# Optimization experiments

Measured on AMD Instinct MI355X. Metric: run time of the kernel, lower is better.

## Reference

```python
import jax, jax.numpy as jnp
import numpy as np

B, S, D, H = 4, 2048, 512, 8
EPS = 1e-5

def _layer_norm(x, gamma, beta):
    mu = jnp.mean(x, axis=-1, keepdims=True)
    var = jnp.mean(jnp.square(x - mu), axis=-1, keepdims=True)
    return (x - mu) * jax.lax.rsqrt(var + EPS) * gamma + beta

def setup_inputs() -> dict:
    key = jax.random.key(0)
    ks = jax.random.split(key, 6)
    sc = 1.0 / np.sqrt(D)
    return {
        "seq_k": jax.random.normal(ks[0], (B, S, D), jnp.float32),
        "seq_q": jax.random.normal(ks[1], (B, S, D), jnp.float32),
        "seq_v": jax.random.normal(ks[2], (B, S, D), jnp.float32),
        "W1": jax.random.normal(ks[3], (D, D), jnp.float32) * sc,
        "W2": jax.random.normal(ks[4], (D, D), jnp.float32) * sc,
        "W3": jax.random.normal(ks[5], (D, D), jnp.float32) * sc,
        "gamma": jnp.ones((D,), jnp.float32),
        "beta": jnp.zeros((D,), jnp.float32),
    }

def reference(seq_k, seq_q, seq_v, W1, W2, W3, gamma, beta):
    # is_layer_norm=True: pre-LN on values; seq_v_value is the normed v
    v_in = _layer_norm(seq_v, gamma, beta)
    # nn.Linear(bias=False): y = x @ W^T
    q = seq_q @ W1.T
    k = seq_k @ W2.T
    v = v_in @ W3.T
    hd = D // H
    q = q.reshape(B, S, H, hd).transpose(0, 2, 1, 3)  # b h s d
    k = k.reshape(B, S, H, hd).transpose(0, 2, 1, 3)
    v = v.reshape(B, S, H, hd).transpose(0, 2, 1, 3)
    # faithful quirk: scores = K @ Q^T, unscaled
    scores = jnp.einsum("bhid,bhjd->bhij", k, q)  # b h s s
    attn = jax.nn.softmax(scores, axis=-1)
    out = jnp.einsum("bhij,bhjd->bhid", attn, v)  # b h s d
    out = out.transpose(0, 2, 1, 3).reshape(B, S, D)
    out = out + v_in                 # is_residual=True
    return _layer_norm(out, gamma, beta)  # final LN
```

## Files before the change

### kernel.cpp

```cpp
#include <hip/hip_runtime.h>
#include <math.h>

#define BB 4
#define SS 2048
#define DD 512
#define HH 8
#define HD 64
#define NTOK (BB*SS)
#define EPS 1e-5f
#define NE ((size_t)NTOK * DD)
#define WN ((size_t)DD * DD)
#define LOG2E 1.4426950408889634f

typedef _Float16 half8v __attribute__((ext_vector_type(8)));
typedef _Float16 half4v __attribute__((ext_vector_type(4)));
typedef _Float16 half2v __attribute__((ext_vector_type(2)));
typedef float f32x4 __attribute__((ext_vector_type(4)));

__device__ __forceinline__ float fast_exp2(float x) {
#if __has_builtin(__builtin_amdgcn_exp2f)
    return __builtin_amdgcn_exp2f(x);
#else
    return __expf(x * 0.6931471805599453f);
#endif
}

__device__ __forceinline__ half2v pack2(float a, float b) {
    return __builtin_bit_cast(half2v, __builtin_amdgcn_cvt_pkrtz(a, b));
}

__device__ __forceinline__ half4v pack4(float a, float b, float c, float d) {
    half2v lo = pack2(a, b);
    half2v hi = pack2(c, d);
    half4v r; r[0] = lo[0]; r[1] = lo[1]; r[2] = hi[0]; r[3] = hi[1];
    return r;
}

__device__ __forceinline__ void gload_lds16(const void* g, void* l) {
    __builtin_amdgcn_global_load_lds(
        (const __attribute__((address_space(1))) unsigned int*)g,
        (__attribute__((address_space(3))) unsigned int*)l, 16, 0, 0);
}

__global__ __launch_bounds__(256) void ln_kernel(const float* __restrict__ x,
                                                 const float* __restrict__ res,
                                                 const float* __restrict__ gamma,
                                                 const float* __restrict__ beta,
                                                 float* __restrict__ y) {
    int row = blockIdx.x;
    const float* xr = x + (size_t)row * DD;
    int t = threadIdx.x;
    float2 v = ((const float2*)xr)[t];
    {
        float2 r = ((const float2*)(res + (size_t)row * DD))[t];
        v.x += r.x; v.y += r.y;
    }
    float s = v.x + v.y;
    float ss = v.x * v.x + v.y * v.y;
    #pragma unroll
    for (int off = 32; off; off >>= 1) {
        s  += __shfl_down(s,  off);
        ss += __shfl_down(ss, off);
    }
    __shared__ float ws0[4], ws1[4];
    int wid = t >> 6, lane = t & 63;
    if (lane == 0) { ws0[wid] = s; ws1[wid] = ss; }
    __syncthreads();
    __shared__ float mu_s, rstd_s;
    if (t == 0) {
        float S0 = ws0[0] + ws0[1] + ws0[2] + ws0[3];
        float S1 = ws1[0] + ws1[1] + ws1[2] + ws1[3];
        float mu = S0 * (1.0f / DD);
        float var = S1 * (1.0f / DD) - mu * mu;
        mu_s = mu;
        rstd_s = rsqrtf(var + EPS);
    }
    __syncthreads();
    float mu = mu_s, rstd = rstd_s;
    float2 g = ((const float2*)gamma)[t];
    float2 bb = ((const float2*)beta)[t];
    float2 o;
    o.x = (v.x - mu) * rstd * g.x + bb.x;
    o.y = (v.y - mu) * rstd * g.y + bb.y;
    ((float2*)(y + (size_t)row * DD))[t] = o;
}

__global__ __launch_bounds__(256) void prep_kernel(const float* __restrict__ seq_v,
                                                   const float* __restrict__ seq_q,
                                                   const float* __restrict__ seq_k,
                                                   const float* __restrict__ W1,
                                                   const float* __restrict__ W2,
                                                   const float* __restrict__ W3,
                                                   const float* __restrict__ gamma,
                                                   const float* __restrict__ beta,
                                                   float* __restrict__ v_in,
                                                   _Float16* __restrict__ v16,
                                                   _Float16* __restrict__ qk16,
                                                   _Float16* __restrict__ w16) {
    int bid = blockIdx.x;
    int t = threadIdx.x;
    if (bid < NTOK) {
        int row = bid;
        float2 v = ((const float2*)(seq_v + (size_t)row * DD))[t];
        float s = v.x + v.y;
        float ss = v.x * v.x + v.y * v.y;
        #pragma unroll
        for (int off = 32; off; off >>= 1) {
            s  += __shfl_down(s,  off);
            ss += __shfl_down(ss, off);
        }
        __shared__ float ws0[4], ws1[4];
        int wid = t >> 6, lane = t & 63;
        if (lane == 0) { ws0[wid] = s; ws1[wid] = ss; }
        __syncthreads();
        __shared__ float mu_s, rstd_s;
        if (t == 0) {
            float S0 = ws0[0] + ws0[1] + ws0[2] + ws0[3];
            float S1 = ws1[0] + ws1[1] + ws1[2] + ws1[3];
            float mu = S0 * (1.0f / DD);
            float var = S1 * (1.0f / DD) - mu * mu;
            mu_s = mu;
            rstd_s = rsqrtf(var + EPS);
        }
        __syncthreads();
        float mu = mu_s, rstd = rstd_s;
        float2 g = ((const float2*)gamma)[t];
        float2 bb = ((const float2*)beta)[t];
        float2 o;
        o.x = (v.x - mu) * rstd * g.x + bb.x;
        o.y = (v.y - mu) * rstd * g.y + bb.y;
        ((float2*)(v_in + (size_t)row * DD))[t] = o;
        *(half2v*)&v16[(size_t)row * DD + 2 * t] = pack2(o.x, o.y);
    } else if (bid < 2 * NTOK) {
        size_t i = ((size_t)(bid - NTOK) * 256 + t) * 4;
        const float* src = (i < NE) ? (seq_q + i) : (seq_k + (i - NE));
        float4 v = *(const float4*)src;
        *(half4v*)(qk16 + i) = pack4(v.x, v.y, v.z, v.w);
    } else {
        size_t i = ((size_t)(bid - 2 * NTOK) * 256 + t) * 4;
        const float* src; float sc;
        if (i < WN)          { src = W1 + i;            sc = LOG2E; }
        else if (i < 2 * WN) { src = W2 + (i - WN);     sc = 1.0f; }
        else                 { src = W3 + (i - 2 * WN); sc = 1.0f; }
        float4 v = *(const float4*)src;
        *(half4v*)(w16 + i) = pack4(v.x * sc, v.y * sc, v.z * sc, v.w * sc);
    }
}

#define GBM 128
#define GBN 128
#define GBK 64
__global__ __launch_bounds__(256) void gemm_mfma(const _Float16* __restrict__ Aall,
                                                 const _Float16* __restrict__ Wall,
                                                 _Float16* __restrict__ Call,
                                                 _Float16* __restrict__ vtOut) {
    __shared__ __align__(16) _Float16 smem[GBM * GBN];
    _Float16* As = smem;
    _Float16* Ws = smem + (size_t)GBM * GBK;
    int z = blockIdx.z;
    bool isv = (z == 2);
    const _Float16* A = Aall + (size_t)z * NE;
    const _Float16* W = Wall + (size_t)z * WN;
    int t = threadIdx.x, w = t >> 6, lane = t & 63, q = lane >> 4, ln = lane & 15;
    int lrow = lane >> 3, lseg = lane & 7;
    int m0 = blockIdx.y * GBM, n0 = blockIdx.x * GBN;
    int wm = w & 1, wn = w >> 1;
    f32x4 acc[4][4];
    #pragma unroll
    for (int mt = 0; mt < 4; ++mt)
        #pragma unroll
        for (int nt = 0; nt < 4; ++nt)
            acc[mt][nt] = (f32x4){0.f, 0.f, 0.f, 0.f};

    int gs = lseg ^ lrow;
    for (int k0 = 0; k0 < DD; k0 += GBK) {
        #pragma unroll
        for (int p = 0; p < 4; ++p) {
            int r = w * 32 + p * 8 + lrow;
            gload_lds16(A + (size_t)(m0 + r) * DD + k0 + gs * 8,
                        As + (size_t)(w * 32 + p * 8) * GBK);
            gload_lds16(W + (size_t)(n0 + r) * DD + k0 + gs * 8,
                        Ws + (size_t)(w * 32 + p * 8) * GBK);
        }
        __syncthreads();
        #pragma unroll
        for (int kk = 0; kk < 2; ++kk) {
            int ch = ((4 * kk + q) ^ (ln & 7)) * 8;
            half8v af[4], wf[4];
            #pragma unroll
            for (int mt = 0; mt < 4; ++mt)
                af[mt] = *(half8v*)&As[(wm * 64 + mt * 16 + ln) * GBK + ch];
            #pragma unroll
            for (int nt = 0; nt < 4; ++nt)
                wf[nt] = *(half8v*)&Ws[(wn * 64 + nt * 16 + ln) * GBK + ch];
            if (!isv) {
                #pragma unroll
                for (int mt = 0; mt < 4; ++mt)
                    #pragma unroll
                    for (int nt = 0; nt < 4; ++nt)
                        acc[mt][nt] = __builtin_amdgcn_mfma_f32_16x16x32_f16(
                            wf[nt], af[mt], acc[mt][nt], 0, 0, 0);
            } else {
                #pragma unroll
                for (int mt = 0; mt < 4; ++mt)
                    #pragma unroll
                    for (int nt = 0; nt < 4; ++nt)
                        acc[mt][nt] = __builtin_amdgcn_mfma_f32_16x16x32_f16(
                            af[mt], wf[nt], acc[mt][nt], 0, 0, 0);
            }
        }
        __syncthreads();
    }

    if (!isv) {
        #pragma unroll
        for (int mt = 0; mt < 4; ++mt) {
            int mloc = wm * 64 + mt * 16 + ln;
            #pragma unroll
            for (int nt = 0; nt < 4; ++nt) {
                int nloc = wn * 64 + nt * 16 + q * 4;
                int cs = (nloc >> 3) ^ (mloc & 7);
                char* p = (char*)smem + mloc * 256 + cs * 16 + (nloc & 7) * 2;
                *(half4v*)p = pack4(acc[mt][nt][0], acc[mt][nt][1],
                                    acc[mt][nt][2], acc[mt][nt][3]);
            }
        }
    } else {
        #pragma unroll
        for (int nt = 0; nt < 4; ++nt) {
            int dloc = wn * 64 + nt * 16 + ln;
            #pragma unroll
            for (int mt = 0; mt < 4; ++mt) {
                int sloc = wm * 64 + mt * 16 + q * 4;
                int cs = (sloc >> 3) ^ (dloc & 7);
                char* p = (char*)smem + dloc * 256 + cs * 16 + (sloc & 7) * 2;
                *(half4v*)p = pack4(acc[mt][nt][0], acc[mt][nt][1],
                                    acc[mt][nt][2], acc[mt][nt][3]);
            }
        }
    }
    __syncthreads();
    int bq = m0 >> 11, sbase = m0 & (SS - 1);
    if (!isv) {
        _Float16* C = Call + (size_t)z * NE;
        #pragma unroll
        for (int p = 0; p < 8; ++p) {
            int id = p * 256 + t;
            int r = id >> 4, c = id & 15;
            half8v vv = *(half8v*)((char*)smem + r * 256 + ((c ^ (r & 7)) * 16));
            int n = n0 + c * 8;
            int h = n >> 6, d0 = n & 63;
            *(half8v*)&C[((size_t)(bq * HH + h) * SS + (sbase + r)) * HD + d0] = vv;
        }
    } else {
        #pragma unroll
        for (int p = 0; p < 8; ++p) {
            int id = p * 256 + t;
            int r = id >> 4, c = id & 15;
            half8v vv = *(half8v*)((char*)smem + r * 256 + ((c ^ (r & 7)) * 16));
            int d = n0 + r;
            int h = d >> 6, dd = d & 63;
            *(half8v*)&vtOut[((size_t)(bq * HH + h) * HD + dd) * SS + sbase + c * 8] = vv;
        }
    }
}

#define AI 128
#define AJ 64
__global__ __launch_bounds__(512, 4) void attn_mfma(const _Float16* __restrict__ qh,
                                                    const _Float16* __restrict__ kh,
                                                    const _Float16* __restrict__ vt,
                                                    float* __restrict__ out) {
    __shared__ __align__(16) _Float16 Qt[2][AJ * HD];
    __shared__ __align__(16) _Float16 Vs[2][HD * AJ];
    __shared__ __align__(16) _Float16 Ps[AI * AJ];
    int t = threadIdx.x, w = t >> 6, lane = t & 63, q = lane >> 4, ln = lane & 15;
    int wg = blockIdx.x;
    int slot = wg >> 3;
    int bh = (wg & 7) * 4 + (slot >> 4);
    int i0 = (slot & 15) * AI;
    int b = bh >> 3, h = bh & 7;
    const _Float16* Kb = kh + (size_t)bh * SS * HD;
    const _Float16* Qb = qh + (size_t)bh * SS * HD;
    const _Float16* Vb = vt + (size_t)bh * HD * SS;

    half8v kf[2];
    #pragma unroll
    for (int kk = 0; kk < 2; ++kk)
        kf[kk] = *(const half8v*)&Kb[(size_t)(i0 + w * 16 + ln) * HD + kk * 32 + q * 8];

    f32x4 oacc[4], lacc;
    float m_run = -3.0e38f;
    lacc = (f32x4){0.f, 0.f, 0.f, 0.f};
    #pragma unroll
    for (int mtd = 0; mtd < 4; ++mtd) oacc[mtd] = (f32x4){0.f, 0.f, 0.f, 0.f};
    half8v ones;
    #pragma unroll
    for (int e = 0; e < 8; ++e) ones[e] = (_Float16)1.0f;
    const f32x4 zf = (f32x4){0.f, 0.f, 0.f, 0.f};

    int sr = t >> 3;
    int sc = t & 7;
    int ssw = sc ^ (sr & 7);

    gload_lds16(Qb + (size_t)sr * HD + ssw * 8, &Qt[0][(size_t)w * 512]);
    gload_lds16(Vb + (size_t)sr * SS + ssw * 8, &Vs[0][(size_t)w * 512]);

    const int NITER = SS / AJ;
    for (int jt = 0; jt < NITER; ++jt) {
        int cur = jt & 1;
        __syncthreads();

        if (jt + 1 < NITER) {
            int j1 = (jt + 1) * AJ;
            gload_lds16(Qb + (size_t)(j1 + sr) * HD + ssw * 8, &Qt[cur ^ 1][(size_t)w * 512]);
            gload_lds16(Vb + (size_t)sr * SS + j1 + ssw * 8,   &Vs[cur ^ 1][(size_t)w * 512]);
        }

        f32x4 sacc[4];
        __builtin_amdgcn_s_setprio(1);
        #pragma unroll
        for (int mt = 0; mt < 4; ++mt) {
            half8v qf = *(half8v*)&Qt[cur][(mt * 16 + ln) * HD + (q ^ (ln & 7)) * 8];
            sacc[mt] = __builtin_amdgcn_mfma_f32_16x16x32_f16(qf, kf[0], zf, 0, 0, 0);
        }
        #pragma unroll
        for (int mt = 0; mt < 4; ++mt) {
            half8v qf = *(half8v*)&Qt[cur][(mt * 16 + ln) * HD + ((4 + q) ^ (ln & 7)) * 8];
            sacc[mt] = __builtin_amdgcn_mfma_f32_16x16x32_f16(qf, kf[1], sacc[mt], 0, 0, 0);
        }
        __builtin_amdgcn_s_setprio(0);

        float mx = fmaxf(fmaxf(sacc[0][0], sacc[0][1]), fmaxf(sacc[0][2], sacc[0][3]));
        #pragma unroll
        for (int mt = 1; mt < 4; ++mt) {
            float m2 = fmaxf(fmaxf(sacc[mt][0], sacc[mt][1]),
                             fmaxf(sacc[mt][2], sacc[mt][3]));
            mx = fmaxf(mx, m2);
        }
        mx = fmaxf(mx, __shfl_xor(mx, 16));
        mx = fmaxf(mx, __shfl_xor(mx, 32));
        if (__any(mx > m_run + 7.0f)) {
            float mn = fmaxf(m_run, mx);
            float a = fast_exp2(m_run - mn);
            lacc *= a;
            #pragma unroll
            for (int mtd = 0; mtd < 4; ++mtd) oacc[mtd] *= a;
            m_run = mn;
        }

        int rp = w * 16 + ln;
        #pragma unroll
        for (int mt = 0; mt < 4; ++mt) {
            float p0 = fast_exp2(sacc[mt][0] - m_run);
            float p1 = fast_exp2(sacc[mt][1] - m_run);
            float p2 = fast_exp2(sacc[mt][2] - m_run);
            float p3 = fast_exp2(sacc[mt][3] - m_run);
            int cw = mt * 2 + (q >> 1);
            int pos = cw ^ (ln & 7);
            *(half4v*)&Ps[(size_t)rp * AJ + pos * 8 + (q & 1) * 4] =
                pack4(p0, p1, p2, p3);
        }

        __builtin_amdgcn_s_setprio(1);
        #pragma unroll
        for (int ks = 0; ks < 2; ++ks) {
            int pos = ((ks * 4 + q) ^ (ln & 7)) * 8;
            half8v pf = *(half8v*)&Ps[(size_t)(w * 16 + ln) * AJ + pos];
            lacc = __builtin_amdgcn_mfma_f32_16x16x32_f16(ones, pf, lacc, 0, 0, 0);
            #pragma unroll
            for (int mtd = 0; mtd < 4; ++mtd) {
                half8v vf = *(half8v*)&Vs[cur][(size_t)(mtd * 16 + ln) * AJ + pos];
                oacc[mtd] = __builtin_amdgcn_mfma_f32_16x16x32_f16(vf, pf, oacc[mtd], 0, 0, 0);
            }
        }
        __builtin_amdgcn_s_setprio(0);
    }

    float inv = 1.0f / lacc[0];
    int i = i0 + w * 16 + ln;
    #pragma unroll
    for (int mtd = 0; mtd < 4; ++mtd) {
        float4 o;
        o.x = oacc[mtd][0] * inv;
        o.y = oacc[mtd][1] * inv;
        o.z = oacc[mtd][2] * inv;
        o.w = oacc[mtd][3] * inv;
        *(float4*)&out[(size_t)(b * SS + i) * DD + h * HD + mtd * 16 + q * 4] = o;
    }
}

extern "C" void kernel_launch(void* const* d_in, const int* in_sizes, int n_in,
                              void* d_out, int out_size, void* d_ws, size_t ws_size,
                              hipStream_t stream) {
    const float* seq_k = (const float*)d_in[0];
    const float* seq_q = (const float*)d_in[1];
    const float* seq_v = (const float*)d_in[2];
    const float* W1    = (const float*)d_in[3];
    const float* W2    = (const float*)d_in[4];
    const float* W3    = (const float*)d_in[5];
    const float* gamma = (const float*)d_in[6];
    const float* beta  = (const float*)d_in[7];
    float* out = (float*)d_out;

    const size_t MB = 1024 * 1024;
    char* w8 = (char*)d_ws;
    float*    v_in = (float*)w8;
    _Float16* a16  = (_Float16*)(w8 + 16 * MB);
    _Float16* w16  = (_Float16*)(w8 + 40 * MB);
    _Float16* qh   = (_Float16*)(w8 + 48 * MB);
    _Float16* vt   = (_Float16*)(w8 + 64 * MB);
    float*    ao   = (float*)(w8 + 16 * MB);

    _Float16* q16 = a16;
    _Float16* v16 = a16 + 2 * NE;
    _Float16* kh  = qh + NE;

    hipLaunchKernelGGL(prep_kernel, dim3(2 * NTOK + 768), dim3(256), 0, stream,
                       seq_v, seq_q, seq_k, W1, W2, W3, gamma, beta,
                       v_in, v16, q16, w16);
    hipLaunchKernelGGL(gemm_mfma, dim3(DD / GBN, NTOK / GBM, 3), dim3(256), 0, stream,
                       a16, w16, qh, vt);
    hipLaunchKernelGGL(attn_mfma, dim3((SS / AI) * BB * HH), dim3(512), 0, stream,
                       qh, kh, vt, ao);
    hipLaunchKernelGGL(ln_kernel, dim3(NTOK), dim3(256), 0, stream,
                       ao, v_in, gamma, beta, out);
}
```

Before: 197.9 us.

## Double-buffer GEMM LDS tiles and remap blocks per XCD

The QKV projection GEMM now double-buffers its LDS tiles. It issues the next k-tile's async global-to-LDS loads before computing on the current one, which cuts the loop to one barrier per iteration. It also raises wave priority around the MFMA section. The 3D grid is flattened into a 1D grid and remapped so that the blocks running on each XCD share A-row tiles, aiming for better L2 reuse. LDS use grows to two stage buffers, and the epilogue reuses buffer 0, so correctness depends on the barrier ordering.

```diff
diff --git a/kernel.cpp b/kernel.cpp
--- a/kernel.cpp
+++ b/kernel.cpp
@@ -154,16 +154,19 @@
                                                  const _Float16* __restrict__ Wall,
                                                  _Float16* __restrict__ Call,
                                                  _Float16* __restrict__ vtOut) {
-    __shared__ __align__(16) _Float16 smem[GBM * GBN];
-    _Float16* As = smem;
-    _Float16* Ws = smem + (size_t)GBM * GBK;
-    int z = blockIdx.z;
+    __shared__ __align__(16) _Float16 smem[2][2 * GBM * GBK];
+    int wg = blockIdx.x;
+    int local = wg >> 3;
+    int z = local >> 5;
+    int r5 = local & 31;
+    int my = (wg & 7) * 8 + (r5 >> 2);
+    int nx = r5 & 3;
     bool isv = (z == 2);
     const _Float16* A = Aall + (size_t)z * NE;
     const _Float16* W = Wall + (size_t)z * WN;
     int t = threadIdx.x, w = t >> 6, lane = t & 63, q = lane >> 4, ln = lane & 15;
     int lrow = lane >> 3, lseg = lane & 7;
-    int m0 = blockIdx.y * GBM, n0 = blockIdx.x * GBN;
+    int m0 = my * GBM, n0 = nx * GBN;
     int wm = w & 1, wn = w >> 1;
     f32x4 acc[4][4];
     #pragma unroll
@@ -173,26 +176,39 @@
             acc[mt][nt] = (f32x4){0.f, 0.f, 0.f, 0.f};
 
     int gs = lseg ^ lrow;
-    for (int k0 = 0; k0 < DD; k0 += GBK) {
+
+    auto stage = [&](int k0, int buf) {
+        _Float16* Asb = smem[buf];
+        _Float16* Wsb = smem[buf] + GBM * GBK;
         #pragma unroll
         for (int p = 0; p < 4; ++p) {
-            int r = w * 32 + p * 8 + lrow;
-            gload_lds16(A + (size_t)(m0 + r) * DD + k0 + gs * 8,
-                        As + (size_t)(w * 32 + p * 8) * GBK);
-            gload_lds16(W + (size_t)(n0 + r) * DD + k0 + gs * 8,
-                        Ws + (size_t)(w * 32 + p * 8) * GBK);
-        }
+            int rr = w * 32 + p * 8 + lrow;
+            gload_lds16(A + (size_t)(m0 + rr) * DD + k0 + gs * 8,
+                        Asb + (size_t)(w * 32 + p * 8) * GBK);
+            gload_lds16(W + (size_t)(n0 + rr) * DD + k0 + gs * 8,
+                        Wsb + (size_t)(w * 32 + p * 8) * GBK);
+        }
+    };
+
+    stage(0, 0);
+    const int NK = DD / GBK;
+    for (int ki = 0; ki < NK; ++ki) {
+        int cur = ki & 1;
         __syncthreads();
+        if (ki + 1 < NK) stage((ki + 1) * GBK, cur ^ 1);
+        _Float16* Asb = smem[cur];
+        _Float16* Wsb = smem[cur] + GBM * GBK;
+        __builtin_amdgcn_s_setprio(1);
         #pragma unroll
         for (int kk = 0; kk < 2; ++kk) {
             int ch = ((4 * kk + q) ^ (ln & 7)) * 8;
             half8v af[4], wf[4];
             #pragma unroll
             for (int mt = 0; mt < 4; ++mt)
-                af[mt] = *(half8v*)&As[(wm * 64 + mt * 16 + ln) * GBK + ch];
+                af[mt] = *(half8v*)&Asb[(wm * 64 + mt * 16 + ln) * GBK + ch];
             #pragma unroll
             for (int nt = 0; nt < 4; ++nt)
-                wf[nt] = *(half8v*)&Ws[(wn * 64 + nt * 16 + ln) * GBK + ch];
+                wf[nt] = *(half8v*)&Wsb[(wn * 64 + nt * 16 + ln) * GBK + ch];
             if (!isv) {
                 #pragma unroll
                 for (int mt = 0; mt < 4; ++mt)
@@ -209,9 +225,10 @@
                             af[mt], wf[nt], acc[mt][nt], 0, 0, 0);
             }
         }
-        __syncthreads();
-    }
-
+        __builtin_amdgcn_s_setprio(0);
+    }
+
+    _Float16* esm = &smem[0][0];
     if (!isv) {
         #pragma unroll
         for (int mt = 0; mt < 4; ++mt) {
@@ -220,7 +237,7 @@
             for (int nt = 0; nt < 4; ++nt) {
                 int nloc = wn * 64 + nt * 16 + q * 4;
                 int cs = (nloc >> 3) ^ (mloc & 7);
-                char* p = (char*)smem + mloc * 256 + cs * 16 + (nloc & 7) * 2;
+                char* p = (char*)esm + mloc * 256 + cs * 16 + (nloc & 7) * 2;
                 *(half4v*)p = pack4(acc[mt][nt][0], acc[mt][nt][1],
                                     acc[mt][nt][2], acc[mt][nt][3]);
             }
@@ -233,7 +250,7 @@
             for (int mt = 0; mt < 4; ++mt) {
                 int sloc = wm * 64 + mt * 16 + q * 4;
                 int cs = (sloc >> 3) ^ (dloc & 7);
-                char* p = (char*)smem + dloc * 256 + cs * 16 + (sloc & 7) * 2;
+                char* p = (char*)esm + dloc * 256 + cs * 16 + (sloc & 7) * 2;
                 *(half4v*)p = pack4(acc[mt][nt][0], acc[mt][nt][1],
                                     acc[mt][nt][2], acc[mt][nt][3]);
             }
@@ -246,19 +263,19 @@
         #pragma unroll
         for (int p = 0; p < 8; ++p) {
             int id = p * 256 + t;
-            int r = id >> 4, c = id & 15;
-            half8v vv = *(half8v*)((char*)smem + r * 256 + ((c ^ (r & 7)) * 16));
+            int rr = id >> 4, c = id & 15;
+            half8v vv = *(half8v*)((char*)esm + rr * 256 + ((c ^ (rr & 7)) * 16));
             int n = n0 + c * 8;
             int h = n >> 6, d0 = n & 63;
-            *(half8v*)&C[((size_t)(bq * HH + h) * SS + (sbase + r)) * HD + d0] = vv;
+            *(half8v*)&C[((size_t)(bq * HH + h) * SS + (sbase + rr)) * HD + d0] = vv;
         }
     } else {
         #pragma unroll
         for (int p = 0; p < 8; ++p) {
             int id = p * 256 + t;
-            int r = id >> 4, c = id & 15;
-            half8v vv = *(half8v*)((char*)smem + r * 256 + ((c ^ (r & 7)) * 16));
-            int d = n0 + r;
+            int rr = id >> 4, c = id & 15;
+            half8v vv = *(half8v*)((char*)esm + rr * 256 + ((c ^ (rr & 7)) * 16));
+            int d = n0 + rr;
             int h = d >> 6, dd = d & 63;
             *(half8v*)&vtOut[((size_t)(bq * HH + h) * HD + dd) * SS + sbase + c * 8] = vv;
         }
@@ -419,7 +436,7 @@
     hipLaunchKernelGGL(prep_kernel, dim3(2 * NTOK + 768), dim3(256), 0, stream,
                        seq_v, seq_q, seq_k, W1, W2, W3, gamma, beta,
                        v_in, v16, q16, w16);
-    hipLaunchKernelGGL(gemm_mfma, dim3(DD / GBN, NTOK / GBM, 3), dim3(256), 0, stream,
+    hipLaunchKernelGGL(gemm_mfma, dim3((DD / GBN) * (NTOK / GBM) * 3), dim3(256), 0, stream,
                        a16, w16, qh, vt);
     hipLaunchKernelGGL(attn_mfma, dim3((SS / AI) * BB * HH), dim3(512), 0, stream,
                        qh, kh, vt, ao);
```

Result: faster. 184.2 us (-6.9%).
